# Kernel tuning notes

Measured on AMD Instinct MI355X. Metric: run time of the kernel, lower is better.

Reference implementation:

```python
import jax, jax.numpy as jnp
import numpy as np

N_NODES = 50000
N_EDGES = 640000
IN_DIM = 128
HID = 128
G_OUT = 128
AX_IN = 64
AX_OUT = 64
OUT_CH = 8
N_GRAPHS = 512


def gcn_conv(x, W, b, src, dst, norm, n_nodes):
    # PyG GCNConv: out = scatter_add(norm * (x W)[src] -> dst) + b
    h = x @ W  # [N, F_out]
    msg = h[src] * norm[:, None]  # [E', F_out]
    return jax.ops.segment_sum(msg, dst, num_segments=n_nodes) + b


def setup_inputs() -> dict:
    key = jax.random.key(0)
    ks = jax.random.split(key, 16)
    inp = {}
    inp["x"] = jax.random.normal(ks[0], (N_NODES, IN_DIM), dtype=jnp.float32)
    inp["edge_index"] = jax.random.randint(ks[1], (2, N_EDGES), 0, N_NODES, dtype=jnp.int64)
    inp["batch"] = jnp.sort(jax.random.randint(ks[2], (N_NODES,), 0, N_GRAPHS, dtype=jnp.int64))
    inp["ax_data"] = jax.random.normal(ks[3], (N_GRAPHS, AX_IN), dtype=jnp.float32)
    def lin(k, fi, fo):
        s = 1.0 / np.sqrt(fi)
        k1, k2 = jax.random.split(k)
        return (jax.random.uniform(k1, (fi, fo), jnp.float32, -s, s),
                jax.random.uniform(k2, (fo,), jnp.float32, -s, s))
    inp["W1"], inp["b1"] = lin(ks[4], IN_DIM, HID)
    inp["W2"], inp["b2"] = lin(ks[5], HID, HID)
    inp["lin1_W"], inp["lin1_b"] = lin(ks[6], HID, G_OUT)
    inp["ax_W"], inp["ax_b"] = lin(ks[7], AX_IN, AX_OUT)
    inp["lin2_W"], inp["lin2_b"] = lin(ks[8], G_OUT + AX_OUT, OUT_CH)
    return inp


def reference(x, edge_index, batch, ax_data, W1, b1, W2, b2, lin1_W, lin1_b, ax_W, ax_b, lin2_W, lin2_b):
    n_nodes = x.shape[0]
    n_graphs = ax_data.shape[0]
    # add self-loops (PyG GCNConv default add_self_loops=True)
    loop = jnp.arange(n_nodes, dtype=edge_index.dtype)
    src = jnp.concatenate([edge_index[0], loop])
    dst = jnp.concatenate([edge_index[1], loop])
    # symmetric normalization D^-1/2 (A+I) D^-1/2
    deg = jax.ops.segment_sum(jnp.ones_like(dst, dtype=x.dtype), dst, num_segments=n_nodes)
    dinv = jax.lax.rsqrt(jnp.maximum(deg, 1.0))  # deg >= 1 with self-loops
    norm = dinv[src] * dinv[dst]  # [E+N]

    h = jax.nn.relu(gcn_conv(x, W1, b1, src, dst, norm, n_nodes))
    h = jax.nn.relu(gcn_conv(h, W2, b2, src, dst, norm, n_nodes))

    # global_mean_pool over batch ids
    sums = jax.ops.segment_sum(h, batch, num_segments=n_graphs)
    cnts = jax.ops.segment_sum(jnp.ones((n_nodes,), h.dtype), batch, num_segments=n_graphs)
    pooled = sums / jnp.maximum(cnts, 1.0)[:, None]  # [G, HID]

    g = pooled @ lin1_W + lin1_b            # [G, G_OUT]
    a = ax_data @ ax_W + ax_b               # [G, AX_OUT]
    z = jnp.concatenate([g, a], axis=1)     # [G, G_OUT+AX_OUT]
    return z @ lin2_W + lin2_b              # [G, OUT_CH]
```

## Files before the change

kernel.cpp:

```cpp
#include <hip/hip_runtime.h>


#define ELLCAP 62
#define BCAP 2048

typedef __attribute__((ext_vector_type(8))) short bf16x8;
typedef __attribute__((ext_vector_type(4))) float f32x4;
typedef __attribute__((ext_vector_type(2))) float f32x2;

static __device__ __forceinline__ unsigned short f2bf(float f) {
  unsigned u = __float_as_uint(f);
  return (unsigned short)((u + 0x7fffu + ((u >> 16) & 1u)) >> 16);
}
static __device__ __forceinline__ unsigned pack2(float a, float b) {
  return (unsigned)f2bf(a) | ((unsigned)f2bf(b) << 16);
}
static __device__ __forceinline__ unsigned char f2fp8(float v) {
  return (unsigned char)(__builtin_amdgcn_cvt_pk_fp8_f32(v, 0.f, 0, false) & 0xff);
}
static __device__ __forceinline__ unsigned enc2(float a, float b) {
  return __builtin_amdgcn_cvt_pk_fp8_f32(a, b, 0, false) & 0xffffu;
}
static __device__ __forceinline__ void add16(float* a, uint4 h) {
  f32x2 t;
  t = __builtin_amdgcn_cvt_pk_f32_fp8(h.x, false); a[0] += t[0]; a[1] += t[1];
  t = __builtin_amdgcn_cvt_pk_f32_fp8(h.x, true);  a[2] += t[0]; a[3] += t[1];
  t = __builtin_amdgcn_cvt_pk_f32_fp8(h.y, false); a[4] += t[0]; a[5] += t[1];
  t = __builtin_amdgcn_cvt_pk_f32_fp8(h.y, true);  a[6] += t[0]; a[7] += t[1];
  t = __builtin_amdgcn_cvt_pk_f32_fp8(h.z, false); a[8] += t[0]; a[9] += t[1];
  t = __builtin_amdgcn_cvt_pk_f32_fp8(h.z, true);  a[10] += t[0]; a[11] += t[1];
  t = __builtin_amdgcn_cvt_pk_f32_fp8(h.w, false); a[12] += t[0]; a[13] += t[1];
  t = __builtin_amdgcn_cvt_pk_f32_fp8(h.w, true);  a[14] += t[0]; a[15] += t[1];
}
static __device__ __forceinline__ uint4 scale16(uint4 h, float d) {
  f32x2 t; float v[16];
  t = __builtin_amdgcn_cvt_pk_f32_fp8(h.x, false); v[0] = d * t[0]; v[1] = d * t[1];
  t = __builtin_amdgcn_cvt_pk_f32_fp8(h.x, true);  v[2] = d * t[0]; v[3] = d * t[1];
  t = __builtin_amdgcn_cvt_pk_f32_fp8(h.y, false); v[4] = d * t[0]; v[5] = d * t[1];
  t = __builtin_amdgcn_cvt_pk_f32_fp8(h.y, true);  v[6] = d * t[0]; v[7] = d * t[1];
  t = __builtin_amdgcn_cvt_pk_f32_fp8(h.z, false); v[8] = d * t[0]; v[9] = d * t[1];
  t = __builtin_amdgcn_cvt_pk_f32_fp8(h.z, true);  v[10] = d * t[0]; v[11] = d * t[1];
  t = __builtin_amdgcn_cvt_pk_f32_fp8(h.w, false); v[12] = d * t[0]; v[13] = d * t[1];
  t = __builtin_amdgcn_cvt_pk_f32_fp8(h.w, true);  v[14] = d * t[0]; v[15] = d * t[1];
  uint4 r;
  r.x = enc2(v[0], v[1]) | (enc2(v[2], v[3]) << 16);
  r.y = enc2(v[4], v[5]) | (enc2(v[6], v[7]) << 16);
  r.z = enc2(v[8], v[9]) | (enc2(v[10], v[11]) << 16);
  r.w = enc2(v[12], v[13]) | (enc2(v[14], v[15]) << 16);
  return r;
}

__global__ void k_wprep(const float* __restrict__ W1, const float* __restrict__ W2,
                        unsigned short* __restrict__ wt1, unsigned short* __restrict__ wt2,
                        unsigned* __restrict__ gcnt, int nb) {
  int b = blockIdx.x, t = threadIdx.x;
  if (b < 128) {
    int idx = b * 256 + t;
    int w = idx >> 14, r = (idx >> 7) & 127, kk = idx & 127;
    if (w == 0) wt1[r * 128 + kk] = f2bf(W1[kk * 128 + r]);
    else        wt2[r * 128 + kk] = f2bf(W2[kk * 128 + r]);
  } else {
    int i = (b - 128) * 256 + t;
    if (i < nb) gcnt[i * 32] = 0;
  }
}

__global__ __launch_bounds__(256, 4) void k_mega1(
    const float* __restrict__ X, const uint4* __restrict__ WT4,
    unsigned char* __restrict__ H8,
    const int* __restrict__ srcv, const int* __restrict__ dstv,
    unsigned* __restrict__ gcnt, unsigned* __restrict__ packed,
    int E, int M, int NG) {
  __shared__ __align__(16) unsigned short sW[64 * 136];
  __shared__ __align__(16) unsigned short sX[64 * 136];
  __shared__ unsigned sbin[392];
  __shared__ unsigned sbase[392];
  int b = blockIdx.x, t = threadIdx.x;
  if (b < NG) {
    int m0 = b * 64;
    const float4* X4 = (const float4*)X;
#pragma unroll
    for (int r = 0; r < 8; r++) {
      int idx = t + r * 256;
      int rr = idx >> 5, c4 = idx & 31;
      int m = m0 + rr;
      float4 v = make_float4(0.f, 0.f, 0.f, 0.f);
      if (m < M) v = X4[(size_t)m * 32 + c4];
      unsigned short* pp = sX + rr * 136 + c4 * 4;
      *(ushort2*)(pp) = make_ushort2(f2bf(v.x), f2bf(v.y));
      *(ushort2*)(pp + 2) = make_ushort2(f2bf(v.z), f2bf(v.w));
    }
    int lane = t & 63, wv = t >> 6;
    int ln15 = lane & 15, q = lane >> 4;
    int r0 = m0 + wv * 16 + q * 4;
    bf16x8 afrag[4];
#pragma unroll
    for (int half = 0; half < 2; half++) {
      if (half) __syncthreads();
#pragma unroll
      for (int r = 0; r < 4; r++) {
        int idx = t + r * 256;
        int nn = idx >> 4, c8 = idx & 15;
        *(uint4*)(sW + nn * 136 + c8 * 8) = WT4[(half * 64 + nn) * 16 + c8];
      }
      __syncthreads();
      if (half == 0) {
#pragma unroll
        for (int c = 0; c < 4; c++)
          afrag[c] = *(const bf16x8*)(sX + (wv * 16 + ln15) * 136 + c * 32 + q * 8);
      }
#pragma unroll
      for (int jj = 0; jj < 4; jj++) {
        int j = half * 4 + jj;
        f32x4 acc = {0.f, 0.f, 0.f, 0.f};
#pragma unroll
        for (int c = 0; c < 4; c++) {
          bf16x8 bfrag = *(const bf16x8*)(sW + (jj * 16 + ln15) * 136 + c * 32 + q * 8);
          acc = __builtin_amdgcn_mfma_f32_16x16x32_bf16(afrag[c], bfrag, acc, 0, 0, 0);
        }
        int col = j * 16 + ln15;
#pragma unroll
        for (int rr = 0; rr < 4; rr++) {
          int m = r0 + rr;
          if (m < M) H8[(size_t)m * 128 + col] = f2fp8(acc[rr]);
        }
      }
    }
  } else {
    int NB = (M + 127) >> 7;
    int e0 = (b - NG) * BCAP;
    int myS[8], myD[8];
#pragma unroll
    for (int j = 0; j < 8; j++) {
      int e = e0 + t + j * 256;
      if (e < E) { myS[j] = srcv[e]; myD[j] = dstv[e]; } else myD[j] = -1;
    }
    for (int i = t; i < NB; i += 256) sbin[i] = 0;
    __syncthreads();
#pragma unroll
    for (int j = 0; j < 8; j++)
      if (myD[j] >= 0) atomicAdd(&sbin[myD[j] >> 7], 1u);
    __syncthreads();
    for (int i = t; i < NB; i += 256) {
      unsigned c = sbin[i];
      sbase[i] = c ? atomicAdd(&gcnt[i * 32], c) : 0u;
    }
    __syncthreads();
    for (int i = t; i < NB; i += 256) sbin[i] = 0;
    __syncthreads();
#pragma unroll
    for (int j = 0; j < 8; j++)
      if (myD[j] >= 0) {
        int bkt = myD[j] >> 7;
        unsigned r = atomicAdd(&sbin[bkt], 1u);
        unsigned pos = sbase[bkt] + r;
        if (pos < BCAP)
          packed[(size_t)bkt * BCAP + pos] =
              (unsigned)myS[j] | ((unsigned)(myD[j] & 127) << 16);
      }
  }
}

__global__ __launch_bounds__(256) void k_ellbuild(const unsigned* __restrict__ packed,
                                                  const unsigned* __restrict__ gcnt,
                                                  unsigned char* __restrict__ ellb,
                                                  int n) {
  __shared__ unsigned short ent[128][ELLCAP];
  __shared__ int ctr[128];
  __shared__ int scnt;
  int b = blockIdx.x, t = threadIdx.x;
  if (t < 128) ctr[t] = 0;
  if (t == 0) scnt = (int)gcnt[b * 32];
  __syncthreads();
  int cnt = scnt; if (cnt > BCAP) cnt = BCAP;
  const unsigned* pk = packed + (size_t)b * BCAP;
  for (int idx = t; idx < cnt; idx += 256) {
    unsigned v = pk[idx];
    int dloc = (int)(v >> 16);
    int slot = atomicAdd(&ctr[dloc], 1);
    if (slot < ELLCAP) ent[dloc][slot] = (unsigned short)(v & 0xffffu);
  }
  __syncthreads();
  int base = b * 128;
#pragma unroll
  for (int p = 0; p < 16; p++) {
    int idx = t + p * 256;
    int i = idx >> 5, u = idx & 31;
    int node = base + i;
    if (node < n) {
      unsigned val;
      if (u == 0) val = (unsigned)ctr[i];
      else {
        int e0 = 2 * u - 2;
        val = (unsigned)ent[i][e0] | ((unsigned)ent[i][e0 + 1] << 16);
      }
      ((unsigned*)ellb)[(size_t)node * 32 + u] = val;
    }
  }
}

__global__ __launch_bounds__(256) void k_scale(unsigned char* __restrict__ ellb,
                                               uint4* __restrict__ H8,
                                               float* __restrict__ dinv, int n) {
  int idx = blockIdx.x * 256 + threadIdx.x;
  int i = idx >> 3, k = idx & 7;
  if (i >= n) return;
  int raw = *(const int*)(ellb + (size_t)i * 128);
  float di = rsqrtf((float)(raw + 1));
  uint4 h = H8[(size_t)i * 8 + k];
  H8[(size_t)i * 8 + k] = scale16(h, di);
  if (k == 0) dinv[i] = di;
}

#define LOADIDX_FULL(S, J)                                             \
  {                                                                    \
    const unsigned* wp_ = (const unsigned*)(row + (J));                \
    unsigned w0_ = wp_[0], w1_ = wp_[1], w2_ = wp_[2], w3_ = wp_[3];   \
    S[0] = (int)(w0_ & 0xffffu); S[1] = (int)(w0_ >> 16);              \
    S[2] = (int)(w1_ & 0xffffu); S[3] = (int)(w1_ >> 16);              \
    S[4] = (int)(w2_ & 0xffffu); S[5] = (int)(w2_ >> 16);              \
    S[6] = (int)(w3_ & 0xffffu); S[7] = (int)(w3_ >> 16);              \
    _Pragma("unroll")                                                  \
    for (int u_ = 1; u_ < 8; u_++)                                     \
      if ((J) + u_ >= deg) S[u_] = S[0];                               \
  }
#define GATHER(H, S)                                                   \
  _Pragma("unroll")                                                    \
  for (int u_ = 0; u_ < 8; u_++) H[u_] = Hs[(size_t)S[u_] * 8 + k];
#define CONSUME(H, J)                                                  \
  _Pragma("unroll")                                                    \
  for (int u_ = 0; u_ < 8; u_++)                                       \
    if ((J) + u_ < deg) add16(acc, H[u_]);

__global__ __launch_bounds__(256) void k_agg(const uint4* __restrict__ Hs,
                                             const unsigned char* __restrict__ ellb,
                                             const float* __restrict__ dinv,
                                             const float* __restrict__ bias,
                                             uint4* __restrict__ Ho, int n) {
  int t = threadIdx.x;
  int oct = t >> 3, k = t & 7;
  int i = blockIdx.x * 32 + oct;
  bool valid = i < n;
  int ic = valid ? i : 0;
  int raw = *(const int*)(ellb + (size_t)ic * 128);
  int deg = raw < ELLCAP ? raw : ELLCAP;
  const unsigned short* row = (const unsigned short*)(ellb + (size_t)ic * 128 + 4);
  float acc[16];
#pragma unroll
  for (int r = 0; r < 16; r++) acc[r] = 0.f;
  uint4 hs = Hs[(size_t)ic * 8 + k];
  add16(acc, hs);
  if (deg > 0) {
    int sA[8], sB[8];
    uint4 hA[8], hB[8];
    int j = 0;
    LOADIDX_FULL(sA, 0);
    GATHER(hA, sA);
    while (true) {
      int jn = j + 8;
      if (jn < deg) { LOADIDX_FULL(sB, jn); GATHER(hB, sB); }
      CONSUME(hA, j);
      j = jn;
      if (j >= deg) break;
      jn = j + 8;
      if (jn < deg) { LOADIDX_FULL(sA, jn); GATHER(hA, sA); }
      CONSUME(hB, j);
      j = jn;
      if (j >= deg) break;
    }
  }
  if (valid) {
    float di = dinv[i];
    const float4* B4 = (const float4*)bias;
    float o[16];
#pragma unroll
    for (int m4 = 0; m4 < 4; m4++) {
      float4 bb = B4[k * 4 + m4];
      o[m4 * 4 + 0] = fmaxf(bb.x + di * acc[m4 * 4 + 0], 0.f);
      o[m4 * 4 + 1] = fmaxf(bb.y + di * acc[m4 * 4 + 1], 0.f);
      o[m4 * 4 + 2] = fmaxf(bb.z + di * acc[m4 * 4 + 2], 0.f);
      o[m4 * 4 + 3] = fmaxf(bb.w + di * acc[m4 * 4 + 3], 0.f);
    }
    uint4 r0, r1;
    r0.x = pack2(o[0], o[1]);   r0.y = pack2(o[2], o[3]);
    r0.z = pack2(o[4], o[5]);   r0.w = pack2(o[6], o[7]);
    r1.x = pack2(o[8], o[9]);   r1.y = pack2(o[10], o[11]);
    r1.z = pack2(o[12], o[13]); r1.w = pack2(o[14], o[15]);
    Ho[(size_t)i * 16 + 2 * k] = r0;
    Ho[(size_t)i * 16 + 2 * k + 1] = r1;
  }
}

__global__ __launch_bounds__(256, 2) void k_gemm2(const unsigned short* __restrict__ Xb,
                                                  const uint4* __restrict__ WT4,
                                                  const float* __restrict__ dinv,
                                                  unsigned char* __restrict__ H8, int M) {
  __shared__ __align__(16) unsigned short sW[128 * 136];
  __shared__ __align__(16) unsigned short sX[64 * 136];
  int tid = threadIdx.x;
  int m0 = blockIdx.x * 64;
#pragma unroll
  for (int r = 0; r < 8; r++) {
    int idx = tid + r * 256;
    int nn = idx >> 4, c8 = idx & 15;
    *(uint4*)(sW + nn * 136 + c8 * 8) = WT4[idx];
  }
  const uint4* X4 = (const uint4*)Xb;
#pragma unroll
  for (int r = 0; r < 4; r++) {
    int idx = tid + r * 256;
    int rr = idx >> 4, c8 = idx & 15;
    int m = m0 + rr;
    uint4 v = make_uint4(0u, 0u, 0u, 0u);
    if (m < M) v = X4[(size_t)m * 16 + c8];
    *(uint4*)(sX + rr * 136 + c8 * 8) = v;
  }
  __syncthreads();
  int lane = tid & 63, wv = tid >> 6;
  int ln15 = lane & 15, q = lane >> 4;
  bf16x8 afrag[4];
#pragma unroll
  for (int c = 0; c < 4; c++)
    afrag[c] = *(const bf16x8*)(sX + (wv * 16 + ln15) * 136 + c * 32 + q * 8);
  int r0 = m0 + wv * 16 + q * 4;
  float dv[4];
#pragma unroll
  for (int rr = 0; rr < 4; rr++) dv[rr] = (r0 + rr < M) ? dinv[r0 + rr] : 0.f;
#pragma unroll
  for (int j = 0; j < 8; j++) {
    f32x4 acc = {0.f, 0.f, 0.f, 0.f};
#pragma unroll
    for (int c = 0; c < 4; c++) {
      bf16x8 bfrag = *(const bf16x8*)(sW + (j * 16 + ln15) * 136 + c * 32 + q * 8);
      acc = __builtin_amdgcn_mfma_f32_16x16x32_bf16(afrag[c], bfrag, acc, 0, 0, 0);
    }
    int col = j * 16 + ln15;
#pragma unroll
    for (int rr = 0; rr < 4; rr++) {
      int m = r0 + rr;
      if (m < M) H8[(size_t)m * 128 + col] = f2fp8(dv[rr] * acc[rr]);
    }
  }
}

__global__ void k_poolhead(const unsigned short* __restrict__ Hb,
                           const int* __restrict__ bat, const float* __restrict__ axd,
                           const float* __restrict__ l1W, const float* __restrict__ l1b,
                           const float* __restrict__ axW, const float* __restrict__ axb,
                           const float* __restrict__ l2W, const float* __restrict__ l2b,
                           float* __restrict__ out, int n) {
  int g = blockIdx.x, t = threadIdx.x;
  __shared__ int sb[2];
  __shared__ float p[128];
  __shared__ float a[64];
  __shared__ float z[192];
  if (t < 2) {
    int target = g + t;
    int lo = 0, hi = n;
    while (lo < hi) {
      int mid = (lo + hi) >> 1;
      if (bat[mid] < target) lo = mid + 1; else hi = mid;
    }
    sb[t] = lo;
  }
  __syncthreads();
  int s = sb[0], e = sb[1];
  int c = e - s; if (c < 1) c = 1;
  float inv = 1.f / (float)c;
  if (t < 128) {
    float s0 = 0.f, s1 = 0.f, s2 = 0.f, s3 = 0.f;
    float s4 = 0.f, s5 = 0.f, s6 = 0.f, s7 = 0.f;
    int r = s;
    for (; r + 8 <= e; r += 8) {
      s0 += __uint_as_float(((unsigned)Hb[(size_t)(r + 0) * 128 + t]) << 16);
      s1 += __uint_as_float(((unsigned)Hb[(size_t)(r + 1) * 128 + t]) << 16);
      s2 += __uint_as_float(((unsigned)Hb[(size_t)(r + 2) * 128 + t]) << 16);
      s3 += __uint_as_float(((unsigned)Hb[(size_t)(r + 3) * 128 + t]) << 16);
      s4 += __uint_as_float(((unsigned)Hb[(size_t)(r + 4) * 128 + t]) << 16);
      s5 += __uint_as_float(((unsigned)Hb[(size_t)(r + 5) * 128 + t]) << 16);
      s6 += __uint_as_float(((unsigned)Hb[(size_t)(r + 6) * 128 + t]) << 16);
      s7 += __uint_as_float(((unsigned)Hb[(size_t)(r + 7) * 128 + t]) << 16);
    }
    for (; r < e; r++)
      s0 += __uint_as_float(((unsigned)Hb[(size_t)r * 128 + t]) << 16);
    p[t] = (((s0 + s1) + (s2 + s3)) + ((s4 + s5) + (s6 + s7))) * inv;
  } else {
    a[t - 128] = axd[g * 64 + (t - 128)];
  }
  __syncthreads();
  if (t < 128) {
    float a0 = 0.f, a1 = 0.f, a2 = 0.f, a3 = 0.f;
#pragma unroll 8
    for (int kk = 0; kk < 128; kk += 4) {
      a0 += p[kk + 0] * l1W[(kk + 0) * 128 + t];
      a1 += p[kk + 1] * l1W[(kk + 1) * 128 + t];
      a2 += p[kk + 2] * l1W[(kk + 2) * 128 + t];
      a3 += p[kk + 3] * l1W[(kk + 3) * 128 + t];
    }
    z[t] = l1b[t] + (a0 + a1) + (a2 + a3);
  } else {
    int j = t - 128;
    float a0 = 0.f, a1 = 0.f, a2 = 0.f, a3 = 0.f;
#pragma unroll 8
    for (int kk = 0; kk < 64; kk += 4) {
      a0 += a[kk + 0] * axW[(kk + 0) * 64 + j];
      a1 += a[kk + 1] * axW[(kk + 1) * 64 + j];
      a2 += a[kk + 2] * axW[(kk + 2) * 64 + j];
      a3 += a[kk + 3] * axW[(kk + 3) * 64 + j];
    }
    z[128 + j] = axb[j] + (a0 + a1) + (a2 + a3);
  }
  __syncthreads();
  if (t < 8) {
    float a0 = 0.f, a1 = 0.f, a2 = 0.f, a3 = 0.f;
#pragma unroll 8
    for (int kk = 0; kk < 192; kk += 4) {
      a0 += z[kk + 0] * l2W[(kk + 0) * 8 + t];
      a1 += z[kk + 1] * l2W[(kk + 1) * 8 + t];
      a2 += z[kk + 2] * l2W[(kk + 2) * 8 + t];
      a3 += z[kk + 3] * l2W[(kk + 3) * 8 + t];
    }
    out[g * 8 + t] = l2b[t] + (a0 + a1) + (a2 + a3);
  }
}

extern "C" void kernel_launch(void* const* d_in, const int* in_sizes, int n_in,
                              void* d_out, int out_size, void* d_ws, size_t ws_size,
                              hipStream_t stream) {
  const float* x   = (const float*)d_in[0];
  const int*   ei  = (const int*)d_in[1];
  const int*   bat = (const int*)d_in[2];
  const float* axd = (const float*)d_in[3];
  const float* W1  = (const float*)d_in[4];
  const float* b1  = (const float*)d_in[5];
  const float* W2  = (const float*)d_in[6];
  const float* b2  = (const float*)d_in[7];
  const float* l1W = (const float*)d_in[8];
  const float* l1b = (const float*)d_in[9];
  const float* axW = (const float*)d_in[10];
  const float* axb = (const float*)d_in[11];
  const float* l2W = (const float*)d_in[12];
  const float* l2b = (const float*)d_in[13];
  float* out = (float*)d_out;

  int n = in_sizes[0] / 128;
  int E = in_sizes[1] / 2;
  int G = in_sizes[3] / 64;
  (void)G;
  int NB = (n + 127) / 128;

  unsigned char* w = (unsigned char*)d_ws;
  unsigned char*  h8    = w;                     w += (size_t)n * 128;
  unsigned short* habuf = (unsigned short*)w;    w += (size_t)n * 128 * 2;
  unsigned short* wt1   = (unsigned short*)w;    w += 16384 * 2;
  unsigned short* wt2   = (unsigned short*)w;    w += 16384 * 2;
  unsigned char*  ellb  = w;                     w += (size_t)n * 128;
  float*    dinv   = (float*)w;                  w += (size_t)n * 4;
  unsigned* gcnt   = (unsigned*)w;               w += (size_t)NB * 128;
  unsigned* packed = (unsigned*)w;               w += (size_t)NB * BCAP * 4;

  const int* srcv = ei;
  const int* dstv = ei + E;
  int NG = (n + 63) / 64;
  int NPB = (E + BCAP - 1) / BCAP;
  int GZ = (NB + 255) / 256;

  k_wprep<<<128 + GZ, 256, 0, stream>>>(W1, W2, wt1, wt2, gcnt, NB);
  k_mega1<<<NG + NPB, 256, 0, stream>>>(x, (const uint4*)wt1, h8, srcv, dstv,
                                        gcnt, packed, E, n, NG);
  k_ellbuild<<<NB, 256, 0, stream>>>(packed, gcnt, ellb, n);
  k_scale<<<(n * 8 + 255) / 256, 256, 0, stream>>>(ellb, (uint4*)h8, dinv, n);
  k_agg<<<(n + 31) / 32, 256, 0, stream>>>((const uint4*)h8, ellb, dinv, b1,
                                           (uint4*)habuf, n);
  k_gemm2<<<NG, 256, 0, stream>>>(habuf, (const uint4*)wt2, dinv, h8, n);
  k_agg<<<(n + 31) / 32, 256, 0, stream>>>((const uint4*)h8, ellb, dinv, b2,
                                           (uint4*)habuf, n);
  k_poolhead<<<512, 192, 0, stream>>>(habuf, bat, axd, l1W, l1b, axW, axb,
                                      l2W, l2b, out, n);
}
```

Measured before the change: 187.3 us.

## Fuse degree scaling into ELL build and unroll aggregation with triple-buffered gathers

```diff
diff --git a/kernel.cpp b/kernel.cpp
--- a/kernel.cpp
+++ b/kernel.cpp
@@ -164,6 +164,8 @@
 __global__ __launch_bounds__(256) void k_ellbuild(const unsigned* __restrict__ packed,
                                                   const unsigned* __restrict__ gcnt,
                                                   unsigned char* __restrict__ ellb,
+                                                  uint4* __restrict__ H8,
+                                                  float* __restrict__ dinv,
                                                   int n) {
   __shared__ unsigned short ent[128][ELLCAP];
   __shared__ int ctr[128];
@@ -197,29 +199,26 @@
       ((unsigned*)ellb)[(size_t)node * 32 + u] = val;
     }
   }
-}
-
-__global__ __launch_bounds__(256) void k_scale(unsigned char* __restrict__ ellb,
-                                               uint4* __restrict__ H8,
-                                               float* __restrict__ dinv, int n) {
-  int idx = blockIdx.x * 256 + threadIdx.x;
-  int i = idx >> 3, k = idx & 7;
-  if (i >= n) return;
-  int raw = *(const int*)(ellb + (size_t)i * 128);
-  float di = rsqrtf((float)(raw + 1));
-  uint4 h = H8[(size_t)i * 8 + k];
-  H8[(size_t)i * 8 + k] = scale16(h, di);
-  if (k == 0) dinv[i] = di;
-}
-
-#define LOADIDX_FULL(S, J)                                             \
+#pragma unroll
+  for (int p = 0; p < 4; p++) {
+    int idx = t + p * 256;
+    int i2 = idx >> 3, kk = idx & 7;
+    int node = base + i2;
+    if (node < n) {
+      float di = rsqrtf((float)(ctr[i2] + 1));
+      uint4 h = H8[(size_t)node * 8 + kk];
+      H8[(size_t)node * 8 + kk] = scale16(h, di);
+      if (kk == 0) dinv[node] = di;
+    }
+  }
+}
+
+#define EXTR(S, wa, wb, wc, wd, J)                                     \
   {                                                                    \
-    const unsigned* wp_ = (const unsigned*)(row + (J));                \
-    unsigned w0_ = wp_[0], w1_ = wp_[1], w2_ = wp_[2], w3_ = wp_[3];   \
-    S[0] = (int)(w0_ & 0xffffu); S[1] = (int)(w0_ >> 16);              \
-    S[2] = (int)(w1_ & 0xffffu); S[3] = (int)(w1_ >> 16);              \
-    S[4] = (int)(w2_ & 0xffffu); S[5] = (int)(w2_ >> 16);              \
-    S[6] = (int)(w3_ & 0xffffu); S[7] = (int)(w3_ >> 16);              \
+    S[0] = (int)((wa) & 0xffffu); S[1] = (int)((wa) >> 16);            \
+    S[2] = (int)((wb) & 0xffffu); S[3] = (int)((wb) >> 16);            \
+    S[4] = (int)((wc) & 0xffffu); S[5] = (int)((wc) >> 16);            \
+    S[6] = (int)((wd) & 0xffffu); S[7] = (int)((wd) >> 16);            \
     _Pragma("unroll")                                                  \
     for (int u_ = 1; u_ < 8; u_++)                                     \
       if ((J) + u_ >= deg) S[u_] = S[0];                               \
@@ -242,35 +241,37 @@
   int i = blockIdx.x * 32 + oct;
   bool valid = i < n;
   int ic = valid ? i : 0;
-  int raw = *(const int*)(ellb + (size_t)ic * 128);
+  const uint4* rp = (const uint4*)(ellb + (size_t)ic * 128);
+  uint4 q0 = rp[0], q1 = rp[1], q2 = rp[2], q3 = rp[3];
+  uint4 hs = Hs[(size_t)ic * 8 + k];
+  float di = dinv[ic];
+  int raw = (int)q0.x;
   int deg = raw < ELLCAP ? raw : ELLCAP;
-  const unsigned short* row = (const unsigned short*)(ellb + (size_t)ic * 128 + 4);
   float acc[16];
 #pragma unroll
   for (int r = 0; r < 16; r++) acc[r] = 0.f;
-  uint4 hs = Hs[(size_t)ic * 8 + k];
+  int sA[8], sB[8], sC[8];
+  uint4 hA[8], hB[8], hC[8];
+  if (deg > 0)  { EXTR(sA, q0.y, q0.z, q0.w, q1.x, 0);  GATHER(hA, sA); }
+  if (deg > 8)  { EXTR(sB, q1.y, q1.z, q1.w, q2.x, 8);  GATHER(hB, sB); }
+  if (deg > 16) { EXTR(sC, q2.y, q2.z, q2.w, q3.x, 16); GATHER(hC, sC); }
+  uint4 q4 = make_uint4(0u, 0u, 0u, 0u), q5 = q4, q6 = q4, q7 = q4;
+  if (deg > 24) { q4 = rp[4]; q5 = rp[5]; q6 = rp[6]; q7 = rp[7]; }
   add16(acc, hs);
-  if (deg > 0) {
-    int sA[8], sB[8];
-    uint4 hA[8], hB[8];
-    int j = 0;
-    LOADIDX_FULL(sA, 0);
-    GATHER(hA, sA);
-    while (true) {
-      int jn = j + 8;
-      if (jn < deg) { LOADIDX_FULL(sB, jn); GATHER(hB, sB); }
-      CONSUME(hA, j);
-      j = jn;
-      if (j >= deg) break;
-      jn = j + 8;
-      if (jn < deg) { LOADIDX_FULL(sA, jn); GATHER(hA, sA); }
-      CONSUME(hB, j);
-      j = jn;
-      if (j >= deg) break;
-    }
-  }
+  if (deg > 0)  CONSUME(hA, 0);
+  if (deg > 24) { EXTR(sA, q3.y, q3.z, q3.w, q4.x, 24); GATHER(hA, sA); }
+  if (deg > 8)  CONSUME(hB, 8);
+  if (deg > 32) { EXTR(sB, q4.y, q4.z, q4.w, q5.x, 32); GATHER(hB, sB); }
+  if (deg > 16) CONSUME(hC, 16);
+  if (deg > 40) { EXTR(sC, q5.y, q5.z, q5.w, q6.x, 40); GATHER(hC, sC); }
+  if (deg > 24) CONSUME(hA, 24);
+  if (deg > 48) { EXTR(sA, q6.y, q6.z, q6.w, q7.x, 48); GATHER(hA, sA); }
+  if (deg > 32) CONSUME(hB, 32);
+  if (deg > 56) { EXTR(sB, q7.y, q7.z, q7.w, q7.w, 56); GATHER(hB, sB); }
+  if (deg > 40) CONSUME(hC, 40);
+  if (deg > 48) CONSUME(hA, 48);
+  if (deg > 56) CONSUME(hB, 56);
   if (valid) {
-    float di = dinv[i];
     const float4* B4 = (const float4*)bias;
     float o[16];
 #pragma unroll
@@ -468,8 +469,7 @@
   k_wprep<<<128 + GZ, 256, 0, stream>>>(W1, W2, wt1, wt2, gcnt, NB);
   k_mega1<<<NG + NPB, 256, 0, stream>>>(x, (const uint4*)wt1, h8, srcv, dstv,
                                         gcnt, packed, E, n, NG);
-  k_ellbuild<<<NB, 256, 0, stream>>>(packed, gcnt, ellb, n);
-  k_scale<<<(n * 8 + 255) / 256, 256, 0, stream>>>(ellb, (uint4*)h8, dinv, n);
+  k_ellbuild<<<NB, 256, 0, stream>>>(packed, gcnt, ellb, (uint4*)h8, dinv, n);
   k_agg<<<(n + 31) / 32, 256, 0, stream>>>((const uint4*)h8, ellb, dinv, b1,
                                            (uint4*)habuf, n);
   k_gemm2<<<NG, 256, 0, stream>>>(habuf, (const uint4*)wt2, dinv, h8, n);
```

New measurement: 186.3 us. About the same (-0.5%).
